# Kernel optimization log

Hardware: AMD Instinct MI355X
Metric: run time of the kernel (lower is better)

The kernel has to match this reference:

```python
import jax, jax.numpy as jnp
import numpy as np

N, E, G = 50000, 400000, 64
DIN, HID, H, ED = 128, 32, 8, 5
HC = H * HID            # 256, conv3 out_channels (concat=False, heads=1)
LH, DOUT = 256, 32
NEG_SLOPE = 0.2


def setup_inputs() -> dict:
    key = jax.random.key(0)
    ks = jax.random.split(key, 32)
    rn = lambda k, s, sc=0.05: (jax.random.normal(k, s, jnp.float32) * sc)
    inp = {
        "x": jax.random.normal(ks[0], (N, DIN), jnp.float32),
        "edge_index": jax.random.randint(ks[1], (2, E), 0, N, jnp.int32),
        "edge_attr": jax.random.uniform(ks[2], (E, ED), jnp.float32),
        "batch": jnp.sort(jax.random.randint(ks[3], (N,), 0, G, jnp.int32)),
        # conv1: in=DIN, heads=H, out=HID, concat=True
        "W1": rn(ks[4], (DIN, H * HID)), "as1": rn(ks[5], (H, HID)), "ad1": rn(ks[6], (H, HID)),
        "We1": rn(ks[7], (ED, H * HID)), "ae1": rn(ks[8], (H, HID)), "b1": jnp.zeros((H * HID,), jnp.float32),
        # conv2: in=H*HID, heads=H, out=HID, concat=True
        "W2": rn(ks[9], (H * HID, H * HID)), "as2": rn(ks[10], (H, HID)), "ad2": rn(ks[11], (H, HID)),
        "We2": rn(ks[12], (ED, H * HID)), "ae2": rn(ks[13], (H, HID)), "b2": jnp.zeros((H * HID,), jnp.float32),
        # conv3: in=H*HID, heads=1, out=HC, concat=False
        "W3": rn(ks[14], (H * HID, HC)), "as3": rn(ks[15], (1, HC)), "ad3": rn(ks[16], (1, HC)),
        "We3": rn(ks[17], (ED, HC)), "ae3": rn(ks[18], (1, HC)), "b3": jnp.zeros((HC,), jnp.float32),
        # MLP head
        "fcW1": rn(ks[19], (HC, LH)), "fcb1": jnp.zeros((LH,), jnp.float32),
        "fcW2": rn(ks[20], (LH, DOUT)), "fcb2": jnp.zeros((DOUT,), jnp.float32),
    }
    return inp


def gat_layer(x, src, dst, ea, W, att_s, att_d, We, att_e, bias, heads, out_ch, concat):
    n = x.shape[0]
    h = (x @ W).reshape(n, heads, out_ch)                 # [N,H,C]
    e = (ea @ We).reshape(-1, heads, out_ch)              # [E,H,C]
    a_s = (h * att_s).sum(-1)                             # [N,H]
    a_d = (h * att_d).sum(-1)                             # [N,H]
    a_e = (e * att_e).sum(-1)                             # [E,H]
    alpha = jax.nn.leaky_relu(a_s[src] + a_d[dst] + a_e, NEG_SLOPE)  # [E,H]
    m = jax.ops.segment_max(alpha, dst, num_segments=n)   # segment softmax over dst
    p = jnp.exp(alpha - m[dst])
    denom = jax.ops.segment_sum(p, dst, num_segments=n)
    w = p / (denom[dst] + 1e-16)                          # [E,H]
    msg = h[src] * w[:, :, None]                          # [E,H,C]
    out = jax.ops.segment_sum(msg, dst, num_segments=n)   # [N,H,C]
    out = out.reshape(n, heads * out_ch) if concat else out.mean(axis=1)
    return out + bias


def reference(x, edge_index, edge_attr, batch,
              W1, as1, ad1, We1, ae1, b1,
              W2, as2, ad2, We2, ae2, b2,
              W3, as3, ad3, We3, ae3, b3,
              fcW1, fcb1, fcW2, fcb2):
    src, dst = edge_index[0], edge_index[1]
    h = jax.nn.elu(gat_layer(x, src, dst, edge_attr, W1, as1, ad1, We1, ae1, b1, H, HID, True))
    h = jax.nn.elu(gat_layer(h, src, dst, edge_attr, W2, as2, ad2, We2, ae2, b2, H, HID, True))
    h = jax.nn.elu(gat_layer(h, src, dst, edge_attr, W3, as3, ad3, We3, ae3, b3, 1, HC, False))
    h = jax.nn.gelu(h @ fcW1 + fcb1, approximate=False) @ fcW2 + fcb2   # [N,DOUT]
    # global_mean_pool over batch ids
    sums = jax.ops.segment_sum(h, batch, num_segments=G)
    cnt = jax.ops.segment_sum(jnp.ones((h.shape[0],), h.dtype), batch, num_segments=G)
    return sums / jnp.maximum(cnt, 1.0)[:, None]
```

## Files before the change

### kernel.cpp

```cpp
#include <hip/hip_runtime.h>
#include <math.h>


#define N_NODES 50000
#define N_EDGES 400000
#define N_GRAPH 64
#define DIN     128
#define NHC     256
#define DOUT    32

typedef _Float16 f16x8 __attribute__((ext_vector_type(8)));
typedef _Float16 f16x4 __attribute__((ext_vector_type(4)));
typedef float    f32x4 __attribute__((ext_vector_type(4)));

#define LDP2 72

__global__ __launch_bounds__(256) void mfma_gemm_kernel(
    const _Float16* __restrict__ Ah, const _Float16* __restrict__ Bh,
    const float* __restrict__ bias, _Float16* __restrict__ Ch,
    const float* __restrict__ asl, const float* __restrict__ adl,
    float* __restrict__ asb, float* __restrict__ adb,
    const int* __restrict__ batch, float* __restrict__ pooled,
    int nrow, int K, int mode)
{
    __shared__ __align__(16) _Float16 sAh[128][LDP2];
    __shared__ __align__(16) _Float16 sBh[64][LDP2];

    const int tid = threadIdx.x, lane = tid & 63, wid = tid >> 6;
    const int wm = wid & 1, wn = wid >> 1;

    int xt, yt;
    if (gridDim.x == 4) {
        int bid = blockIdx.x + (blockIdx.y << 2);
        yt = (bid >> 5) * 8 + (bid & 7);
        xt = (bid >> 3) & 3;
    } else { xt = blockIdx.x; yt = blockIdx.y; }
    const int row0 = yt * 128, col0 = xt * 64;
    if (row0 >= nrow) return;

    const int frow = lane & 15, fk = (lane >> 4) * 8;

    f32x4 acc[4][2] = {};
    f16x8 pA[4], pB[2];

#pragma unroll
    for (int p = 0; p < 4; p++) {
        int idx = tid + p * 256;
        int r = idx >> 3, ch = (idx & 7) * 8;
        int gr = row0 + r;
        pA[p] = (gr < nrow) ? *(const f16x8*)(Ah + (long)gr * K + ch) : (f16x8)0;
    }
#pragma unroll
    for (int p = 0; p < 2; p++) {
        int idx = tid + p * 256;
        int r = idx >> 3, ch = (idx & 7) * 8;
        pB[p] = *(const f16x8*)(Bh + (long)(col0 + r) * K + ch);
    }

    for (int k0 = 0; k0 < K; k0 += 64) {
#pragma unroll
        for (int p = 0; p < 4; p++) {
            int idx = tid + p * 256;
            *(f16x8*)&sAh[idx >> 3][(idx & 7) * 8] = pA[p];
        }
#pragma unroll
        for (int p = 0; p < 2; p++) {
            int idx = tid + p * 256;
            *(f16x8*)&sBh[idx >> 3][(idx & 7) * 8] = pB[p];
        }
        __syncthreads();

        if (k0 + 64 < K) {
            int kn = k0 + 64;
#pragma unroll
            for (int p = 0; p < 4; p++) {
                int idx = tid + p * 256;
                int r = idx >> 3, ch = (idx & 7) * 8;
                int gr = row0 + r;
                pA[p] = (gr < nrow) ? *(const f16x8*)(Ah + (long)gr * K + kn + ch) : (f16x8)0;
            }
#pragma unroll
            for (int p = 0; p < 2; p++) {
                int idx = tid + p * 256;
                int r = idx >> 3, ch = (idx & 7) * 8;
                pB[p] = *(const f16x8*)(Bh + (long)(col0 + r) * K + kn + ch);
            }
        }

#pragma unroll
        for (int sub = 0; sub < 2; sub++) {
            const int fks = fk + sub * 32;
            f16x8 bh[2];
#pragma unroll
            for (int nt = 0; nt < 2; nt++)
                bh[nt] = *(const f16x8*)&sBh[wn * 32 + nt * 16 + frow][fks];
#pragma unroll
            for (int mt = 0; mt < 4; mt++) {
                f16x8 ah = *(const f16x8*)&sAh[wm * 64 + mt * 16 + frow][fks];
#pragma unroll
                for (int nt = 0; nt < 2; nt++)
                    acc[mt][nt] = __builtin_amdgcn_mfma_f32_16x16x32_f16(ah, bh[nt], acc[mt][nt], 0, 0, 0);
            }
        }
        __syncthreads();
    }

    const int crow0 = row0 + wm * 64 + (lane >> 4) * 4;
    const int ccol0 = col0 + wn * 32 + (lane & 15);

    if (mode == 0) {
#pragma unroll
        for (int mt = 0; mt < 4; mt++)
#pragma unroll
            for (int nt = 0; nt < 2; nt++) {
                int col = ccol0 + nt * 16;
#pragma unroll
                for (int r = 0; r < 4; r++) {
                    int row = crow0 + mt * 16 + r;
                    if (row < nrow) Ch[(long)row * 256 + col] = (_Float16)acc[mt][nt][r];
                }
            }
        if (asl != nullptr) {
            const float asl0 = asl[ccol0], asl1 = asl[ccol0 + 16];
            const float adl0 = adl[ccol0], adl1 = adl[ccol0 + 16];
            const int headw = (col0 + wn * 32) >> 5;
#pragma unroll
            for (int mt = 0; mt < 4; mt++) {
#pragma unroll
                for (int r = 0; r < 4; r++) {
                    float s = acc[mt][0][r] * asl0 + acc[mt][1][r] * asl1;
                    float d = acc[mt][0][r] * adl0 + acc[mt][1][r] * adl1;
                    s += __shfl_xor(s, 1); s += __shfl_xor(s, 2);
                    s += __shfl_xor(s, 4); s += __shfl_xor(s, 8);
                    d += __shfl_xor(d, 1); d += __shfl_xor(d, 2);
                    d += __shfl_xor(d, 4); d += __shfl_xor(d, 8);
                    if ((lane & 15) == 0) {
                        int row = crow0 + mt * 16 + r;
                        if (row < nrow) {
                            asb[row * 8 + headw] = s;
                            adb[row * 8 + headw] = d;
                        }
                    }
                }
            }
        }
    } else {
        float* pool = (float*)&sAh[0][0];
        const int g0 = batch[row0];
        const int rlast = (row0 + 127 < nrow) ? row0 + 127 : nrow - 1;
        const int gspan = batch[rlast] - g0 + 1;
        const bool fits = (gspan <= 16);
        for (int i = tid; i < 16 * 64; i += 256) pool[i] = 0.f;
        __syncthreads();

        const float b0 = bias[ccol0], b1 = bias[ccol0 + 16];
        const int lc0 = ccol0 - col0, lc1 = lc0 + 16;
        float sum0 = 0.f, sum1 = 0.f;
        int curg = -1;
#pragma unroll
        for (int mt = 0; mt < 4; mt++) {
#pragma unroll
            for (int r = 0; r < 4; r++) {
                int row = crow0 + mt * 16 + r;
                if (row >= nrow) continue;
                int g = batch[row];
                if (g != curg) {
                    if (curg >= 0) {
                        if (fits) {
                            atomicAdd(&pool[(curg - g0) * 64 + lc0], sum0);
                            atomicAdd(&pool[(curg - g0) * 64 + lc1], sum1);
                        } else {
                            atomicAdd(&pooled[curg * 256 + ccol0], sum0);
                            atomicAdd(&pooled[curg * 256 + ccol0 + 16], sum1);
                        }
                    }
                    curg = g; sum0 = 0.f; sum1 = 0.f;
                }
                float v0 = acc[mt][0][r] + b0;
                float v1 = acc[mt][1][r] + b1;
                sum0 += 0.5f * v0 * (1.f + erff(v0 * 0.7071067811865475f));
                sum1 += 0.5f * v1 * (1.f + erff(v1 * 0.7071067811865475f));
            }
        }
        if (curg >= 0) {
            if (fits) {
                atomicAdd(&pool[(curg - g0) * 64 + lc0], sum0);
                atomicAdd(&pool[(curg - g0) * 64 + lc1], sum1);
            } else {
                atomicAdd(&pooled[curg * 256 + ccol0], sum0);
                atomicAdd(&pooled[curg * 256 + ccol0 + 16], sum1);
            }
        }
        __syncthreads();
        if (fits) {
            for (int i = tid; i < gspan * 64; i += 256) {
                float val = pool[i];
                if (val != 0.f)
                    atomicAdd(&pooled[(g0 + (i >> 6)) * 256 + col0 + (i & 63)], val);
            }
        }
    }
}

#define J0 1600000
#define J1 32768
#define J2 65536
#define J3 65536
#define J4 65536
#define J5 16384
#define J6 N_NODES
#define J7 64
#define JTOT (J0+J1+J2+J3+J4+J5+J6+J7)

__device__ __forceinline__ void t_one(const float* W, _Float16* Bh,
                                      int id, int K, int realN)
{
    int n = id / K, k = id - n * K;
    Bh[id] = (_Float16)W[(long)k * realN + n];
}

__global__ __launch_bounds__(256) void prep_kernel(
    const float* __restrict__ x,
    const float* __restrict__ W1, const float* __restrict__ W2, const float* __restrict__ W3,
    const float* __restrict__ F1,
    _Float16* __restrict__ xh,
    _Float16* __restrict__ W1th, _Float16* __restrict__ W2th,
    _Float16* __restrict__ W3th, _Float16* __restrict__ F1th,
    float* __restrict__ pooled, int* __restrict__ deg, int* __restrict__ gcnt)
{
    int idx = blockIdx.x * 256 + threadIdx.x;
    if (idx < J0) {
        float4 v = ((const float4*)x)[idx];
        f16x4 h;
        h[0] = (_Float16)v.x; h[1] = (_Float16)v.y;
        h[2] = (_Float16)v.z; h[3] = (_Float16)v.w;
        *(f16x4*)(xh + (long)idx * 4) = h;
        return;
    }
    idx -= J0;
    if (idx < J1) { t_one(W1, W1th, idx, DIN, NHC); return; }
    idx -= J1;
    if (idx < J2) { t_one(W2, W2th, idx, NHC, NHC); return; }
    idx -= J2;
    if (idx < J3) { t_one(W3, W3th, idx, NHC, NHC); return; }
    idx -= J3;
    if (idx < J4) { t_one(F1, F1th, idx, NHC, NHC); return; }
    idx -= J4;
    if (idx < J5) { pooled[idx] = 0.f; return; }
    idx -= J5;
    if (idx < J6) { deg[idx] = 0; return; }
    idx -= J6;
    if (idx < J7) { gcnt[idx] = 0; return; }
}

__global__ void me_all_kernel(
    const float* __restrict__ We1, const float* __restrict__ ae1,
    const float* __restrict__ We2, const float* __restrict__ ae2,
    const float* __restrict__ We3, const float* __restrict__ ae3,
    float* __restrict__ MeAll)
{
    int l = blockIdx.x;
    const float* We = (l == 0) ? We1 : (l == 1) ? We2 : We3;
    const float* ae = (l == 0) ? ae1 : (l == 1) ? ae2 : ae3;
    int H = (l == 2) ? 1 : 8, C = (l == 2) ? 256 : 32;
    int t = threadIdx.x;
    if (t >= 5 * H) return;
    int j = t / H, hh = t - j * H;
    float s = 0.f;
    for (int c = 0; c < C; c++) s += We[j * NHC + hh * C + c] * ae[hh * C + c];
    MeAll[l * 40 + j * H + hh] = s;
}

__global__ __launch_bounds__(256) void asd_kernel(
    const _Float16* __restrict__ h, const float* __restrict__ atts, const float* __restrict__ attd,
    float* __restrict__ asb, float* __restrict__ adb, int total)
{
    int n = blockIdx.x * 256 + threadIdx.x;
    if (n >= total) return;
    const f16x8* hp = (const f16x8*)(h + (long)n * NHC);
    const float4* sp = (const float4*)atts;
    const float4* dp = (const float4*)attd;
    float ss = 0.f, dd = 0.f;
    for (int c = 0; c < NHC / 8; c++) {
        f16x8 hv = hp[c];
        float4 s1 = sp[2 * c], s2 = sp[2 * c + 1];
        float4 d1 = dp[2 * c], d2 = dp[2 * c + 1];
        ss += (float)hv[0] * s1.x + (float)hv[1] * s1.y + (float)hv[2] * s1.z + (float)hv[3] * s1.w
            + (float)hv[4] * s2.x + (float)hv[5] * s2.y + (float)hv[6] * s2.z + (float)hv[7] * s2.w;
        dd += (float)hv[0] * d1.x + (float)hv[1] * d1.y + (float)hv[2] * d1.z + (float)hv[3] * d1.w
            + (float)hv[4] * d2.x + (float)hv[5] * d2.y + (float)hv[6] * d2.z + (float)hv[7] * d2.w;
    }
    asb[n * 8] = ss; adb[n * 8] = dd;
}

__global__ __launch_bounds__(256) void count_hist_kernel(
    const int* __restrict__ ei, const int* __restrict__ batch,
    int* __restrict__ deg, int* __restrict__ gcnt, int E, int N)
{
    __shared__ int hist[N_GRAPH];
    int t = threadIdx.x;
    if (t < N_GRAPH) hist[t] = 0;
    __syncthreads();
    int i = blockIdx.x * 256 + t;
    if (i < E) atomicAdd(&deg[ei[E + i]], 1);
    if (i < N) atomicAdd(&hist[batch[i]], 1);
    __syncthreads();
    if (t < N_GRAPH && hist[t] > 0) atomicAdd(&gcnt[t], hist[t]);
}

__global__ __launch_bounds__(256) void scan_block_kernel(
    const int* __restrict__ deg, int* __restrict__ rowstart, int* __restrict__ partial, int n)
{
    __shared__ int s[256];
    int i = blockIdx.x * 256 + threadIdx.x;
    int v = (i < n) ? deg[i] : 0;
    s[threadIdx.x] = v;
    __syncthreads();
    for (int off = 1; off < 256; off <<= 1) {
        int t = (threadIdx.x >= off) ? s[threadIdx.x - off] : 0;
        __syncthreads();
        s[threadIdx.x] += t;
        __syncthreads();
    }
    if (i < n) rowstart[i] = s[threadIdx.x] - v;
    if (threadIdx.x == 255) partial[blockIdx.x] = s[255];
}

__global__ __launch_bounds__(256) void scan_partial_kernel(int* __restrict__ partial, int nb)
{
    __shared__ int s[256];
    int v = (threadIdx.x < nb) ? partial[threadIdx.x] : 0;
    s[threadIdx.x] = v;
    __syncthreads();
    for (int off = 1; off < 256; off <<= 1) {
        int t = (threadIdx.x >= off) ? s[threadIdx.x - off] : 0;
        __syncthreads();
        s[threadIdx.x] += t;
        __syncthreads();
    }
    if (threadIdx.x < nb) partial[threadIdx.x] = s[threadIdx.x] - v;
}

__global__ __launch_bounds__(256) void scan_add_kernel(
    int* __restrict__ rowstart, const int* __restrict__ partial, int* __restrict__ cursor,
    int n, int E)
{
    int i = blockIdx.x * 256 + threadIdx.x;
    if (i < n) {
        int v = rowstart[i] + partial[blockIdx.x];
        rowstart[i] = v;
        cursor[i] = v;
    }
    if (i == 0) rowstart[n] = E;
}

__global__ __launch_bounds__(256) void fill_kernel(
    const int* __restrict__ ei, int* __restrict__ cursor, int2* __restrict__ csr2, int E)
{
    int e = blockIdx.x * 256 + threadIdx.x;
    if (e >= E) return;
    int dst = ei[E + e];
    int pos = atomicAdd(&cursor[dst], 1);
    csr2[pos] = make_int2(ei[e], e);
}

__global__ __launch_bounds__(256) void aec_kernel(
    const int2* __restrict__ csr2, const float* __restrict__ ea,
    const float* __restrict__ MeAll,
    int* __restrict__ csr, _Float16* __restrict__ aec, int E)
{
    int pos = blockIdx.x * 256 + threadIdx.x;
    if (pos >= E) return;
    int2 se = csr2[pos];
    csr[pos] = se.x;
    const float* eap = ea + (long)se.y * 5;
    float e0 = eap[0], e1 = eap[1], e2 = eap[2], e3 = eap[3], e4 = eap[4];
#pragma unroll
    for (int l = 0; l < 2; l++) {
        const float* Me = MeAll + l * 40;
        f16x8 v;
#pragma unroll
        for (int hh = 0; hh < 8; hh++) {
            float s = e0 * Me[hh] + e1 * Me[8 + hh] + e2 * Me[16 + hh]
                    + e3 * Me[24 + hh] + e4 * Me[32 + hh];
            v[hh] = (_Float16)s;
        }
        *(f16x8*)(aec + (long)l * N_EDGES * 8 + (long)pos * 8) = v;
    }
    const float* Me2 = MeAll + 80;
    float s2 = e0 * Me2[0] + e1 * Me2[1] + e2 * Me2[2] + e3 * Me2[3] + e4 * Me2[4];
    f16x8 v2;
#pragma unroll
    for (int hh = 0; hh < 8; hh++) v2[hh] = (_Float16)s2;
    *(f16x8*)(aec + (long)2 * N_EDGES * 8 + (long)pos * 8) = v2;
}

__global__ __launch_bounds__(256) void gat_agg_kernel(
    const int* __restrict__ rowstart, const int* __restrict__ csr,
    const _Float16* __restrict__ aec, const float* __restrict__ asb,
    const float* __restrict__ adb,
    const _Float16* __restrict__ h, const float* __restrict__ bias,
    _Float16* __restrict__ Oh, int H, int clog2)
{
    int node = blockIdx.x * 4 + (threadIdx.x >> 6);
    if (node >= N_NODES) return;
    const int lane = threadIdx.x & 63;
    const int half = lane >> 5;
    const int c8   = (lane & 31) * 8;
    const int hc   = c8 >> clog2;
    const int heff = lane & (H - 1);
    const int grp  = lane >> 3;

    const float adn = adb[node * 8 + heff];
    const int beg = rowstart[node], end = rowstart[node + 1];

    float acc[8] = {};
    float den = 0.f;

    for (int i = beg; i < end; i += 8) {
        int idx = i + grp;
        const bool valid = (idx < end);
        if (!valid) idx = end - 1;
        const int sj = csr[idx];
        const float ae = (float)aec[(long)idx * 8 + heff];
        float al = asb[sj * 8 + heff] + adn + ae;
        al = fmaxf(al, 0.2f * al);
        const float pv = valid ? __expf(al) : 0.f;
#pragma unroll
        for (int jj = 0; jj < 4; jj++) {
            const int j = jj * 2 + half;
            const float pj = __shfl(pv, j * 8 + hc);
            const int srcj = __shfl(sj, j * 8);
            const f16x8 hv = *(const f16x8*)(h + (long)srcj * NHC + c8);
            den += pj;
#pragma unroll
            for (int k = 0; k < 8; k++)
                acc[k] += pj * (float)hv[k];
        }
    }

    den += __shfl_xor(den, 32);
#pragma unroll
    for (int k = 0; k < 8; k++)
        acc[k] += __shfl_xor(acc[k], 32);

    if (half == 0) {
        const float w = 1.0f / (den + 1e-16f);
        const float4 b0 = *(const float4*)(bias + c8);
        const float4 b1 = *(const float4*)(bias + c8 + 4);
        const float bb[8] = {b0.x, b0.y, b0.z, b0.w, b1.x, b1.y, b1.z, b1.w};
        f16x8 oh;
#pragma unroll
        for (int k = 0; k < 8; k++) {
            float v = acc[k] * w + bb[k];
            v = (v > 0.f) ? v : (__expf(v) - 1.f);
            oh[k] = (_Float16)v;
        }
        *(f16x8*)(Oh + (long)node * NHC + c8) = oh;
    }
}

__global__ void final_kernel(const float* __restrict__ pooled, const int* __restrict__ gcnt,
                             const float* __restrict__ fcW2, const float* __restrict__ fcb2,
                             float* __restrict__ out)
{
    int g = blockIdx.x;
    int j = threadIdx.x;
    if (j >= DOUT) return;
    float s = 0.f;
    for (int k = 0; k < NHC; k++) s += pooled[g * NHC + k] * fcW2[k * DOUT + j];
    int c = gcnt[g];
    out[g * DOUT + j] = (c > 0) ? (s / (float)c + fcb2[j]) : 0.f;
}

extern "C" void kernel_launch(void* const* d_in, const int* in_sizes, int n_in,
                              void* d_out, int out_size, void* d_ws, size_t ws_size,
                              hipStream_t stream)
{
    const float* x    = (const float*)d_in[0];
    const int*   ei   = (const int*)  d_in[1];
    const float* ea   = (const float*)d_in[2];
    const int*   bat  = (const int*)  d_in[3];
    const float* W[3]   = {(const float*)d_in[4],  (const float*)d_in[10], (const float*)d_in[16]};
    const float* Asl[3] = {(const float*)d_in[5],  (const float*)d_in[11], (const float*)d_in[17]};
    const float* Adl[3] = {(const float*)d_in[6],  (const float*)d_in[12], (const float*)d_in[18]};
    const float* Wel[3] = {(const float*)d_in[7],  (const float*)d_in[13], (const float*)d_in[19]};
    const float* Ael[3] = {(const float*)d_in[8],  (const float*)d_in[14], (const float*)d_in[20]};
    const float* Bil[3] = {(const float*)d_in[9],  (const float*)d_in[15], (const float*)d_in[21]};
    const float* fcW1 = (const float*)d_in[22];
    const float* fcb1 = (const float*)d_in[23];
    const float* fcW2 = (const float*)d_in[24];
    const float* fcb2 = (const float*)d_in[25];

    char* w = (char*)d_ws;
    _Float16* h    = (_Float16*)w;     w += (size_t)N_NODES * NHC * 2;
    _Float16* xh   = (_Float16*)w;     w += (size_t)N_NODES * DIN * 2;
    _Float16* xbh  = (_Float16*)w;     w += (size_t)N_NODES * NHC * 2;
    float*    asb  = (float*)w;        w += (size_t)N_NODES * 8 * 4;
    float*    adb  = (float*)w;        w += (size_t)N_NODES * 8 * 4;
    float*    MeAll= (float*)w;        w += 120 * 4;
    float*    pooled=(float*)w;        w += (size_t)N_GRAPH * NHC * 4;
    _Float16* W1th = (_Float16*)w;     w += (size_t)NHC * DIN * 2;
    _Float16* W2th = (_Float16*)w;     w += (size_t)NHC * NHC * 2;
    _Float16* W3th = (_Float16*)w;     w += (size_t)NHC * NHC * 2;
    _Float16* F1th = (_Float16*)w;     w += (size_t)NHC * NHC * 2;
    int* gcnt     = (int*)w;           w += N_GRAPH * 4;
    int* deg      = (int*)w;           w += (size_t)N_NODES * 4;
    int* rowstart = (int*)w;           w += (size_t)(N_NODES + 1) * 4;
    int* cursor   = (int*)w;           w += (size_t)N_NODES * 4;
    int* partial  = (int*)w;           w += 256 * 4;
    w = (char*)(((size_t)w + 15) & ~(size_t)15);
    int2* csr2    = (int2*)w;          w += (size_t)N_EDGES * 8;
    int* csr      = (int*)w;           w += (size_t)N_EDGES * 4;
    w = (char*)(((size_t)w + 15) & ~(size_t)15);
    _Float16* aec = (_Float16*)w;      w += (size_t)3 * N_EDGES * 8 * 2;

    const int NB = (N_NODES + 255) / 256;

    prep_kernel<<<(JTOT + 255) / 256, 256, 0, stream>>>(
        x, W[0], W[1], W[2], fcW1,
        xh, W1th, W2th, W3th, F1th,
        pooled, deg, gcnt);
    count_hist_kernel<<<(N_EDGES + 255) / 256, 256, 0, stream>>>(ei, bat, deg, gcnt, N_EDGES, N_NODES);
    scan_block_kernel<<<NB, 256, 0, stream>>>(deg, rowstart, partial, N_NODES);
    scan_partial_kernel<<<1, 256, 0, stream>>>(partial, NB);
    scan_add_kernel<<<NB, 256, 0, stream>>>(rowstart, partial, cursor, N_NODES, N_EDGES);
    me_all_kernel<<<3, 64, 0, stream>>>(Wel[0], Ael[0], Wel[1], Ael[1], Wel[2], Ael[2], MeAll);
    fill_kernel<<<(N_EDGES + 255) / 256, 256, 0, stream>>>(ei, cursor, csr2, N_EDGES);
    aec_kernel<<<(N_EDGES + 255) / 256, 256, 0, stream>>>(csr2, ea, MeAll, csr, aec, N_EDGES);

    const int Hs[3] = {8, 8, 1};
    const int CL[3] = {5, 5, 8};
    const int Ks[3] = {DIN, NHC, NHC};

    const dim3 ggrid(4, 392);

    const _Float16* curh = xh;
    const _Float16* Wth[3] = {W1th, W2th, W3th};
    for (int l = 0; l < 3; l++) {
        const int H = Hs[l];
        const bool fuse = (l != 2);
        mfma_gemm_kernel<<<ggrid, 256, 0, stream>>>(
            curh, Wth[l], nullptr, h,
            fuse ? Asl[l] : nullptr, fuse ? Adl[l] : nullptr, asb, adb,
            nullptr, nullptr,
            N_NODES, Ks[l], 0);
        if (!fuse)
            asd_kernel<<<(N_NODES + 255) / 256, 256, 0, stream>>>(
                h, Asl[l], Adl[l], asb, adb, N_NODES);
        gat_agg_kernel<<<(N_NODES + 3) / 4, 256, 0, stream>>>(
            rowstart, csr, aec + (size_t)l * N_EDGES * 8, asb, adb, h, Bil[l], xbh, H, CL[l]);
        curh = xbh;
    }

    mfma_gemm_kernel<<<ggrid, 256, 0, stream>>>(
        xbh, F1th, fcb1, nullptr,
        nullptr, nullptr, nullptr, nullptr,
        bat, pooled,
        N_NODES, NHC, 3);
    final_kernel<<<N_GRAPH, 64, 0, stream>>>(pooled, gcnt, fcW2, fcb2, (float*)d_out);
}
```

Baseline: 428.2 us.

## Retile GEMM to full-width 64-row blocks and fuse single-head attention scores

The MFMA GEMM changes from 128x64 tiles to 64x256 tiles, so each block computes every output column of its rows and each wave owns 64 columns. Because of this, the layer-3 single-head attention dot products can be reduced inside the block through shared memory, and the separate asd_kernel pass that re-read h is removed. The pooled GELU epilogue now covers all 256 columns per block. The cost is a larger B tile in shared memory (about 46 KB per block), more accumulator registers per thread, and a launch-bounds hint asking for three blocks per SM.

```diff
diff --git a/kernel.cpp b/kernel.cpp
--- a/kernel.cpp
+++ b/kernel.cpp
@@ -15,56 +15,48 @@
 
 #define LDP2 72
 
-__global__ __launch_bounds__(256) void mfma_gemm_kernel(
+__global__ __launch_bounds__(256, 3) void mfma_gemm_kernel(
     const _Float16* __restrict__ Ah, const _Float16* __restrict__ Bh,
     const float* __restrict__ bias, _Float16* __restrict__ Ch,
     const float* __restrict__ asl, const float* __restrict__ adl,
     float* __restrict__ asb, float* __restrict__ adb,
     const int* __restrict__ batch, float* __restrict__ pooled,
-    int nrow, int K, int mode)
-{
-    __shared__ __align__(16) _Float16 sAh[128][LDP2];
-    __shared__ __align__(16) _Float16 sBh[64][LDP2];
-
-    const int tid = threadIdx.x, lane = tid & 63, wid = tid >> 6;
-    const int wm = wid & 1, wn = wid >> 1;
-
-    int xt, yt;
-    if (gridDim.x == 4) {
-        int bid = blockIdx.x + (blockIdx.y << 2);
-        yt = (bid >> 5) * 8 + (bid & 7);
-        xt = (bid >> 3) & 3;
-    } else { xt = blockIdx.x; yt = blockIdx.y; }
-    const int row0 = yt * 128, col0 = xt * 64;
+    int nrow, int K, int nheads, int mode)
+{
+    __shared__ __align__(16) _Float16 sAh[64][LDP2];
+    __shared__ __align__(16) _Float16 sBh[256][LDP2];
+
+    const int tid = threadIdx.x, lane = tid & 63, wn = tid >> 6;
+    const int row0 = blockIdx.x * 64;
     if (row0 >= nrow) return;
 
     const int frow = lane & 15, fk = (lane >> 4) * 8;
 
-    f32x4 acc[4][2] = {};
-    f16x8 pA[4], pB[2];
-
-#pragma unroll
-    for (int p = 0; p < 4; p++) {
+    f32x4 acc[4][4] = {};
+    f16x8 pA[2], pB[8];
+
+#pragma unroll
+    for (int p = 0; p < 2; p++) {
         int idx = tid + p * 256;
         int r = idx >> 3, ch = (idx & 7) * 8;
         int gr = row0 + r;
         pA[p] = (gr < nrow) ? *(const f16x8*)(Ah + (long)gr * K + ch) : (f16x8)0;
     }
 #pragma unroll
-    for (int p = 0; p < 2; p++) {
+    for (int p = 0; p < 8; p++) {
         int idx = tid + p * 256;
         int r = idx >> 3, ch = (idx & 7) * 8;
-        pB[p] = *(const f16x8*)(Bh + (long)(col0 + r) * K + ch);
+        pB[p] = *(const f16x8*)(Bh + (long)r * K + ch);
     }
 
     for (int k0 = 0; k0 < K; k0 += 64) {
 #pragma unroll
-        for (int p = 0; p < 4; p++) {
+        for (int p = 0; p < 2; p++) {
             int idx = tid + p * 256;
             *(f16x8*)&sAh[idx >> 3][(idx & 7) * 8] = pA[p];
         }
 #pragma unroll
-        for (int p = 0; p < 2; p++) {
+        for (int p = 0; p < 8; p++) {
             int idx = tid + p * 256;
             *(f16x8*)&sBh[idx >> 3][(idx & 7) * 8] = pB[p];
         }
@@ -73,46 +65,46 @@
         if (k0 + 64 < K) {
             int kn = k0 + 64;
 #pragma unroll
-            for (int p = 0; p < 4; p++) {
+            for (int p = 0; p < 2; p++) {
                 int idx = tid + p * 256;
                 int r = idx >> 3, ch = (idx & 7) * 8;
                 int gr = row0 + r;
                 pA[p] = (gr < nrow) ? *(const f16x8*)(Ah + (long)gr * K + kn + ch) : (f16x8)0;
             }
 #pragma unroll
-            for (int p = 0; p < 2; p++) {
+            for (int p = 0; p < 8; p++) {
                 int idx = tid + p * 256;
                 int r = idx >> 3, ch = (idx & 7) * 8;
-                pB[p] = *(const f16x8*)(Bh + (long)(col0 + r) * K + kn + ch);
+                pB[p] = *(const f16x8*)(Bh + (long)r * K + kn + ch);
             }
         }
 
 #pragma unroll
         for (int sub = 0; sub < 2; sub++) {
             const int fks = fk + sub * 32;
-            f16x8 bh[2];
-#pragma unroll
-            for (int nt = 0; nt < 2; nt++)
-                bh[nt] = *(const f16x8*)&sBh[wn * 32 + nt * 16 + frow][fks];
-#pragma unroll
-            for (int mt = 0; mt < 4; mt++) {
-                f16x8 ah = *(const f16x8*)&sAh[wm * 64 + mt * 16 + frow][fks];
-#pragma unroll
-                for (int nt = 0; nt < 2; nt++)
-                    acc[mt][nt] = __builtin_amdgcn_mfma_f32_16x16x32_f16(ah, bh[nt], acc[mt][nt], 0, 0, 0);
-            }
-        }
-        __syncthreads();
-    }
-
-    const int crow0 = row0 + wm * 64 + (lane >> 4) * 4;
-    const int ccol0 = col0 + wn * 32 + (lane & 15);
+            f16x8 ah[4];
+#pragma unroll
+            for (int mt = 0; mt < 4; mt++)
+                ah[mt] = *(const f16x8*)&sAh[mt * 16 + frow][fks];
+#pragma unroll
+            for (int nt = 0; nt < 4; nt++) {
+                f16x8 bh = *(const f16x8*)&sBh[wn * 64 + nt * 16 + frow][fks];
+#pragma unroll
+                for (int mt = 0; mt < 4; mt++)
+                    acc[mt][nt] = __builtin_amdgcn_mfma_f32_16x16x32_f16(ah[mt], bh, acc[mt][nt], 0, 0, 0);
+            }
+        }
+        __syncthreads();
+    }
+
+    const int crow0 = row0 + (lane >> 4) * 4;
+    const int ccol0 = wn * 64 + (lane & 15);
 
     if (mode == 0) {
 #pragma unroll
         for (int mt = 0; mt < 4; mt++)
 #pragma unroll
-            for (int nt = 0; nt < 2; nt++) {
+            for (int nt = 0; nt < 4; nt++) {
                 int col = ccol0 + nt * 16;
 #pragma unroll
                 for (int r = 0; r < 4; r++) {
@@ -121,41 +113,88 @@
                 }
             }
         if (asl != nullptr) {
-            const float asl0 = asl[ccol0], asl1 = asl[ccol0 + 16];
-            const float adl0 = adl[ccol0], adl1 = adl[ccol0 + 16];
-            const int headw = (col0 + wn * 32) >> 5;
-#pragma unroll
-            for (int mt = 0; mt < 4; mt++) {
-#pragma unroll
-                for (int r = 0; r < 4; r++) {
-                    float s = acc[mt][0][r] * asl0 + acc[mt][1][r] * asl1;
-                    float d = acc[mt][0][r] * adl0 + acc[mt][1][r] * adl1;
-                    s += __shfl_xor(s, 1); s += __shfl_xor(s, 2);
-                    s += __shfl_xor(s, 4); s += __shfl_xor(s, 8);
-                    d += __shfl_xor(d, 1); d += __shfl_xor(d, 2);
-                    d += __shfl_xor(d, 4); d += __shfl_xor(d, 8);
-                    if ((lane & 15) == 0) {
-                        int row = crow0 + mt * 16 + r;
-                        if (row < nrow) {
-                            asb[row * 8 + headw] = s;
-                            adb[row * 8 + headw] = d;
+            if (nheads == 8) {
+                const float asl0 = asl[ccol0],      asl1 = asl[ccol0 + 16];
+                const float asl2 = asl[ccol0 + 32], asl3 = asl[ccol0 + 48];
+                const float adl0 = adl[ccol0],      adl1 = adl[ccol0 + 16];
+                const float adl2 = adl[ccol0 + 32], adl3 = adl[ccol0 + 48];
+#pragma unroll
+                for (int mt = 0; mt < 4; mt++) {
+#pragma unroll
+                    for (int r = 0; r < 4; r++) {
+                        float s0 = acc[mt][0][r] * asl0 + acc[mt][1][r] * asl1;
+                        float s1 = acc[mt][2][r] * asl2 + acc[mt][3][r] * asl3;
+                        float d0 = acc[mt][0][r] * adl0 + acc[mt][1][r] * adl1;
+                        float d1 = acc[mt][2][r] * adl2 + acc[mt][3][r] * adl3;
+                        s0 += __shfl_xor(s0, 1); s0 += __shfl_xor(s0, 2);
+                        s0 += __shfl_xor(s0, 4); s0 += __shfl_xor(s0, 8);
+                        s1 += __shfl_xor(s1, 1); s1 += __shfl_xor(s1, 2);
+                        s1 += __shfl_xor(s1, 4); s1 += __shfl_xor(s1, 8);
+                        d0 += __shfl_xor(d0, 1); d0 += __shfl_xor(d0, 2);
+                        d0 += __shfl_xor(d0, 4); d0 += __shfl_xor(d0, 8);
+                        d1 += __shfl_xor(d1, 1); d1 += __shfl_xor(d1, 2);
+                        d1 += __shfl_xor(d1, 4); d1 += __shfl_xor(d1, 8);
+                        if ((lane & 15) == 0) {
+                            int row = crow0 + mt * 16 + r;
+                            if (row < nrow) {
+                                asb[row * 8 + wn * 2]     = s0;
+                                asb[row * 8 + wn * 2 + 1] = s1;
+                                adb[row * 8 + wn * 2]     = d0;
+                                adb[row * 8 + wn * 2 + 1] = d1;
+                            }
                         }
                     }
                 }
+            } else {
+                float* red = (float*)&sAh[0][0];
+                const float a0 = asl[ccol0],      a1 = asl[ccol0 + 16];
+                const float a2 = asl[ccol0 + 32], a3 = asl[ccol0 + 48];
+                const float b0 = adl[ccol0],      b1 = adl[ccol0 + 16];
+                const float b2 = adl[ccol0 + 32], b3 = adl[ccol0 + 48];
+#pragma unroll
+                for (int mt = 0; mt < 4; mt++) {
+#pragma unroll
+                    for (int r = 0; r < 4; r++) {
+                        float s = acc[mt][0][r] * a0 + acc[mt][1][r] * a1
+                                + acc[mt][2][r] * a2 + acc[mt][3][r] * a3;
+                        float d = acc[mt][0][r] * b0 + acc[mt][1][r] * b1
+                                + acc[mt][2][r] * b2 + acc[mt][3][r] * b3;
+                        s += __shfl_xor(s, 1); s += __shfl_xor(s, 2);
+                        s += __shfl_xor(s, 4); s += __shfl_xor(s, 8);
+                        d += __shfl_xor(d, 1); d += __shfl_xor(d, 2);
+                        d += __shfl_xor(d, 4); d += __shfl_xor(d, 8);
+                        if ((lane & 15) == 0) {
+                            int rl = (lane >> 4) * 4 + mt * 16 + r;
+                            red[rl * 8 + wn]     = s;
+                            red[rl * 8 + 4 + wn] = d;
+                        }
+                    }
+                }
+                __syncthreads();
+                if (tid < 64) {
+                    int row = row0 + tid;
+                    if (row < nrow) {
+                        float s = red[tid * 8] + red[tid * 8 + 1] + red[tid * 8 + 2] + red[tid * 8 + 3];
+                        float d = red[tid * 8 + 4] + red[tid * 8 + 5] + red[tid * 8 + 6] + red[tid * 8 + 7];
+                        asb[row * 8] = s;
+                        adb[row * 8] = d;
+                    }
+                }
             }
         }
     } else {
-        float* pool = (float*)&sAh[0][0];
+        float* pool = (float*)&sBh[0][0];
         const int g0 = batch[row0];
-        const int rlast = (row0 + 127 < nrow) ? row0 + 127 : nrow - 1;
+        const int rlast = (row0 + 63 < nrow) ? row0 + 63 : nrow - 1;
         const int gspan = batch[rlast] - g0 + 1;
         const bool fits = (gspan <= 16);
-        for (int i = tid; i < 16 * 64; i += 256) pool[i] = 0.f;
-        __syncthreads();
-
-        const float b0 = bias[ccol0], b1 = bias[ccol0 + 16];
-        const int lc0 = ccol0 - col0, lc1 = lc0 + 16;
-        float sum0 = 0.f, sum1 = 0.f;
+        for (int i = tid; i < 16 * 256; i += 256) pool[i] = 0.f;
+        __syncthreads();
+
+        float bb[4];
+#pragma unroll
+        for (int nt = 0; nt < 4; nt++) bb[nt] = bias[ccol0 + nt * 16];
+        float sums[4] = {};
         int curg = -1;
 #pragma unroll
         for (int mt = 0; mt < 4; mt++) {
@@ -167,36 +206,42 @@
                 if (g != curg) {
                     if (curg >= 0) {
                         if (fits) {
-                            atomicAdd(&pool[(curg - g0) * 64 + lc0], sum0);
-                            atomicAdd(&pool[(curg - g0) * 64 + lc1], sum1);
+#pragma unroll
+                            for (int nt = 0; nt < 4; nt++)
+                                atomicAdd(&pool[(curg - g0) * 256 + ccol0 + nt * 16], sums[nt]);
                         } else {
-                            atomicAdd(&pooled[curg * 256 + ccol0], sum0);
-                            atomicAdd(&pooled[curg * 256 + ccol0 + 16], sum1);
+#pragma unroll
+                            for (int nt = 0; nt < 4; nt++)
+                                atomicAdd(&pooled[curg * 256 + ccol0 + nt * 16], sums[nt]);
                         }
                     }
-                    curg = g; sum0 = 0.f; sum1 = 0.f;
+                    curg = g;
+                    sums[0] = sums[1] = sums[2] = sums[3] = 0.f;
                 }
-                float v0 = acc[mt][0][r] + b0;
-                float v1 = acc[mt][1][r] + b1;
-                sum0 += 0.5f * v0 * (1.f + erff(v0 * 0.7071067811865475f));
-                sum1 += 0.5f * v1 * (1.f + erff(v1 * 0.7071067811865475f));
+#pragma unroll
+                for (int nt = 0; nt < 4; nt++) {
+                    float v = acc[mt][nt][r] + bb[nt];
+                    sums[nt] += 0.5f * v * (1.f + erff(v * 0.7071067811865475f));
+                }
             }
         }
         if (curg >= 0) {
             if (fits) {
-                atomicAdd(&pool[(curg - g0) * 64 + lc0], sum0);
-                atomicAdd(&pool[(curg - g0) * 64 + lc1], sum1);
+#pragma unroll
+                for (int nt = 0; nt < 4; nt++)
+                    atomicAdd(&pool[(curg - g0) * 256 + ccol0 + nt * 16], sums[nt]);
             } else {
-                atomicAdd(&pooled[curg * 256 + ccol0], sum0);
-                atomicAdd(&pooled[curg * 256 + ccol0 + 16], sum1);
+#pragma unroll
+                for (int nt = 0; nt < 4; nt++)
+                    atomicAdd(&pooled[curg * 256 + ccol0 + nt * 16], sums[nt]);
             }
         }
         __syncthreads();
         if (fits) {
-            for (int i = tid; i < gspan * 64; i += 256) {
+            for (int i = tid; i < gspan * 256; i += 256) {
                 float val = pool[i];
                 if (val != 0.f)
-                    atomicAdd(&pooled[(g0 + (i >> 6)) * 256 + col0 + (i & 63)], val);
+                    atomicAdd(&pooled[(g0 + (i >> 8)) * 256 + (i & 255)], val);
             }
         }
     }
@@ -269,28 +314,6 @@
     float s = 0.f;
     for (int c = 0; c < C; c++) s += We[j * NHC + hh * C + c] * ae[hh * C + c];
     MeAll[l * 40 + j * H + hh] = s;
-}
-
-__global__ __launch_bounds__(256) void asd_kernel(
-    const _Float16* __restrict__ h, const float* __restrict__ atts, const float* __restrict__ attd,
-    float* __restrict__ asb, float* __restrict__ adb, int total)
-{
-    int n = blockIdx.x * 256 + threadIdx.x;
-    if (n >= total) return;
-    const f16x8* hp = (const f16x8*)(h + (long)n * NHC);
-    const float4* sp = (const float4*)atts;
-    const float4* dp = (const float4*)attd;
-    float ss = 0.f, dd = 0.f;
-    for (int c = 0; c < NHC / 8; c++) {
-        f16x8 hv = hp[c];
-        float4 s1 = sp[2 * c], s2 = sp[2 * c + 1];
-        float4 d1 = dp[2 * c], d2 = dp[2 * c + 1];
-        ss += (float)hv[0] * s1.x + (float)hv[1] * s1.y + (float)hv[2] * s1.z + (float)hv[3] * s1.w
-            + (float)hv[4] * s2.x + (float)hv[5] * s2.y + (float)hv[6] * s2.z + (float)hv[7] * s2.w;
-        dd += (float)hv[0] * d1.x + (float)hv[1] * d1.y + (float)hv[2] * d1.z + (float)hv[3] * d1.w
-            + (float)hv[4] * d2.x + (float)hv[5] * d2.y + (float)hv[6] * d2.z + (float)hv[7] * d2.w;
-    }
-    asb[n * 8] = ss; adb[n * 8] = dd;
 }
 
 __global__ __launch_bounds__(256) void count_hist_kernel(
@@ -516,6 +539,7 @@
     _Float16* aec = (_Float16*)w;      w += (size_t)3 * N_EDGES * 8 * 2;
 
     const int NB = (N_NODES + 255) / 256;
+    const int GB = (N_NODES + 63) / 64;
 
     prep_kernel<<<(JTOT + 255) / 256, 256, 0, stream>>>(
         x, W[0], W[1], W[2], fcW1,
@@ -533,30 +557,24 @@
     const int CL[3] = {5, 5, 8};
     const int Ks[3] = {DIN, NHC, NHC};
 
-    const dim3 ggrid(4, 392);
-
     const _Float16* curh = xh;
     const _Float16* Wth[3] = {W1th, W2th, W3th};
     for (int l = 0; l < 3; l++) {
         const int H = Hs[l];
-        const bool fuse = (l != 2);
-        mfma_gemm_kernel<<<ggrid, 256, 0, stream>>>(
+        mfma_gemm_kernel<<<GB, 256, 0, stream>>>(
             curh, Wth[l], nullptr, h,
-            fuse ? Asl[l] : nullptr, fuse ? Adl[l] : nullptr, asb, adb,
+            Asl[l], Adl[l], asb, adb,
             nullptr, nullptr,
-            N_NODES, Ks[l], 0);
-        if (!fuse)
-            asd_kernel<<<(N_NODES + 255) / 256, 256, 0, stream>>>(
-                h, Asl[l], Adl[l], asb, adb, N_NODES);
+            N_NODES, Ks[l], H, 0);
         gat_agg_kernel<<<(N_NODES + 3) / 4, 256, 0, stream>>>(
             rowstart, csr, aec + (size_t)l * N_EDGES * 8, asb, adb, h, Bil[l], xbh, H, CL[l]);
         curh = xbh;
     }
 
-    mfma_gemm_kernel<<<ggrid, 256, 0, stream>>>(
+    mfma_gemm_kernel<<<GB, 256, 0, stream>>>(
         xbh, F1th, fcb1, nullptr,
         nullptr, nullptr, nullptr, nullptr,
         bat, pooled,
-        N_NODES, NHC, 3);
+        N_NODES, NHC, 0, 3);
     final_kernel<<<N_GRAPH, 64, 0, stream>>>(pooled, gcnt, fcW2, fcb2, (float*)d_out);
 }
```

New measurement: 444.5 us. 1.04x slower.
